# Kernel tuning notes

Hardware: AMD Instinct MI355X
Metric: run time of the kernel (lower is better)

The kernel has to match this reference:

```python
import jax, jax.numpy as jnp
import numpy as np

N_NODES = 10000
N_EDGES = 320000
N_GRAPHS = 64


def _gcn_conv(x, edge_index, W, b, n):
    # PyG GCNConv: add self-loops, symmetric deg^-1/2 normalization, x@W, scatter-add at target, + bias
    loop = jnp.arange(n)
    src = jnp.concatenate([edge_index[0], loop])
    dst = jnp.concatenate([edge_index[1], loop])
    deg = jax.ops.segment_sum(jnp.ones_like(dst, dtype=x.dtype), dst, num_segments=n)
    dinv = jnp.where(deg > 0, 1.0 / jnp.sqrt(jnp.maximum(deg, 1.0)), 0.0)
    norm = dinv[src] * dinv[dst]            # [E']
    h = x @ W                               # [N, out]
    out = jax.ops.segment_sum(h[src] * norm[:, None], dst, num_segments=n)
    return out + b


def _mean_pool(x, batch, g):
    s = jax.ops.segment_sum(x, batch, num_segments=g)
    cnt = jax.ops.segment_sum(jnp.ones((x.shape[0],), x.dtype), batch, num_segments=g)
    return s / jnp.maximum(cnt, 1.0)[:, None]


def setup_inputs() -> dict:
    key = jax.random.key(0)
    ks = jax.random.split(key, 20)
    x = jax.random.normal(ks[0], (N_NODES, 1), dtype=jnp.float32)
    edge_index = jax.random.randint(ks[1], (2, N_EDGES), 0, N_NODES, dtype=jnp.int64)
    batch = jnp.sort(jax.random.randint(ks[2], (N_NODES,), 0, N_GRAPHS, dtype=jnp.int64))

    def lin(k, fi, fo):
        k1, k2 = jax.random.split(k)
        lim = 1.0 / np.sqrt(fi)
        W = jax.random.uniform(k1, (fi, fo), jnp.float32, -lim, lim)
        b = jax.random.uniform(k2, (fo,), jnp.float32, -lim, lim)
        return W, b

    W1, b1 = lin(ks[3], 1, 256)
    W2, b2 = lin(ks[4], 256, 256)
    W3, b3 = lin(ks[5], 256, 128)
    W4, b4 = lin(ks[6], 128, 128)
    W5, b5 = lin(ks[7], 128, 64)
    W6, b6 = lin(ks[8], 64, 32)
    W7, b7 = lin(ks[9], 32, 1)
    return dict(x=x, edge_index=edge_index, batch=batch,
                W1=W1, b1=b1, W2=W2, b2=b2, W3=W3, b3=b3, W4=W4, b4=b4,
                W5=W5, b5=b5, W6=W6, b6=b6, W7=W7, b7=b7)


def reference(x, edge_index, batch, W1, b1, W2, b2, W3, b3, W4, b4, W5, b5, W6, b6, W7, b7):
    n = x.shape[0]
    h = jax.nn.relu(_gcn_conv(x, edge_index, W1, b1, n))
    h = jax.nn.relu(_gcn_conv(h, edge_index, W2, b2, n))
    g = _mean_pool(h, batch, N_GRAPHS)          # [G, 256]
    g = jax.nn.relu(g @ W3 + b3)
    g = jax.nn.relu(g @ W4 + b4)
    g = jax.nn.relu(g @ W5 + b5)
    g = jax.nn.relu(g @ W6 + b6)
    y = (g @ W7 + b7).reshape(-1)               # [G]
    return y
```

## Files before the change

kernel.cpp:

```cpp
#include <hip/hip_runtime.h>

#define N_NODES  10000
#define N_EDGES  320000
#define N_GRAPHS 64
#define F 256
#define POOL_SPLIT 8


__global__ void k_prep(const int* batch, int* cnti, float* s, int* gstart) {
    int i = blockIdx.x * blockDim.x + threadIdx.x;
    if (i >= N_NODES) return;
    cnti[i] = 0;
    s[i] = 0.0f;
    int b = batch[i];
    if (i == 0) {
        for (int g = 0; g <= b; g++) gstart[g] = 0;
    } else {
        int bp = batch[i - 1];
        for (int g = bp + 1; g <= b; g++) gstart[g] = i;
    }
    if (i == N_NODES - 1) {
        for (int g = b + 1; g <= N_GRAPHS; g++) gstart[g] = N_NODES;
    }
}

__global__ void k_deg(const int* dst, int* cnti) {
    int e = blockIdx.x * blockDim.x + threadIdx.x;
    if (e < N_EDGES) atomicAdd(&cnti[dst[e]], 1);
}

__global__ void k_scan(const int* cnti, int* offs, int* cursor, float* dinv) {
    __shared__ int part[256];
    int t = threadIdx.x;
    const int CH = 40;
    int lo = t * CH, hi = lo + CH;
    if (hi > N_NODES) hi = N_NODES;
    if (lo > N_NODES) lo = N_NODES;
    int sum = 0;
    for (int i = lo; i < hi; i++) sum += cnti[i];
    part[t] = sum;
    __syncthreads();
    for (int off = 1; off < 256; off <<= 1) {
        int v = (t >= off) ? part[t - off] : 0;
        __syncthreads();
        if (t >= off) part[t] += v;
        __syncthreads();
    }
    int base = (t == 0) ? 0 : part[t - 1];
    for (int i = lo; i < hi; i++) {
        offs[i] = base; cursor[i] = base; base += cnti[i];
        dinv[i] = 1.0f / sqrtf((float)(cnti[i] + 1));
    }
}

__global__ void k_edge(const int* src, const int* dst, const float* x,
                       const float* dinv, int* cursor, int* csr, float* s) {
    int e = blockIdx.x * blockDim.x + threadIdx.x;
    if (e >= N_EDGES) return;
    int sv = src[e], dv = dst[e];
    int pos = atomicAdd(&cursor[dv], 1);
    csr[pos] = sv;
    atomicAdd(&s[dv], dinv[sv] * x[sv]);
}

__global__ void k_sfin(const float* s, const float* dinv, const float* x, float2* sd) {
    int i = blockIdx.x * blockDim.x + threadIdx.x;
    if (i >= N_NODES) return;
    float di = dinv[i];
    sd[i] = make_float2(di * (s[i] + di * x[i]), di);
}

#define EDGE_TERM(t)                                  \
    acc.x += fmaxf(fmaf((t).x, w.x, bv.x), 0.f) * (t).y; \
    acc.y += fmaxf(fmaf((t).x, w.y, bv.y), 0.f) * (t).y; \
    acc.z += fmaxf(fmaf((t).x, w.z, bv.z), 0.f) * (t).y; \
    acc.w += fmaxf(fmaf((t).x, w.w, bv.w), 0.f) * (t).y;

__global__ __launch_bounds__(256) void k_agg(const float2* sd, const float* W1, const float* b1,
                                             const int* offs, const int* cnti, const int* csr,
                                             float* agg) {
    int wid  = (blockIdx.x * blockDim.x + threadIdx.x) >> 6;
    int lane = threadIdx.x & 63;
    if (wid >= N_NODES) return;
    float4 w  = ((const float4*)W1)[lane];
    float4 bv = ((const float4*)b1)[lane];
    float2 self = sd[wid];
    float4 acc = {0.f, 0.f, 0.f, 0.f};
    EDGE_TERM(self)
    int lo = offs[wid], n = cnti[wid];
    int j = 0;
    for (; j + 3 < n; j += 4) {
        int s0 = csr[lo + j],     s1 = csr[lo + j + 1];
        int s2 = csr[lo + j + 2], s3 = csr[lo + j + 3];
        float2 t0 = sd[s0], t1 = sd[s1], t2 = sd[s2], t3 = sd[s3];
        EDGE_TERM(t0) EDGE_TERM(t1) EDGE_TERM(t2) EDGE_TERM(t3)
    }
    for (; j < n; j++) {
        float2 t = sd[csr[lo + j]];
        EDGE_TERM(t)
    }
    float di = self.y;
    float4 o; o.x = acc.x * di; o.y = acc.y * di; o.z = acc.z * di; o.w = acc.w * di;
    ((float4*)(agg + (size_t)wid * F))[lane] = o;
}

__global__ __launch_bounds__(256) void k_gemm(const float* A, const float* B,
                                              const float* bias, float* C) {
    __shared__ float As[16][68];
    __shared__ float Bs[16][64];
    int tid  = threadIdx.x;
    int row0 = blockIdx.x * 64;
    int col0 = blockIdx.y * 64;
    float acc[4][4] = {};
    int am = tid >> 2, ak = (tid & 3) * 4;
    int bk = tid >> 4, bn = (tid & 15) * 4;
    int ty = tid >> 4, tx = tid & 15;
    for (int k0 = 0; k0 < 256; k0 += 16) {
        float4 av = {0.f, 0.f, 0.f, 0.f};
        if (row0 + am < N_NODES)
            av = *(const float4*)(A + (size_t)(row0 + am) * 256 + k0 + ak);
        As[ak + 0][am] = av.x; As[ak + 1][am] = av.y;
        As[ak + 2][am] = av.z; As[ak + 3][am] = av.w;
        float4 bvv = *(const float4*)(B + (size_t)(k0 + bk) * 256 + col0 + bn);
        *(float4*)&Bs[bk][bn] = bvv;
        __syncthreads();
        #pragma unroll
        for (int k = 0; k < 16; k++) {
            float4 a4 = *(const float4*)&As[k][ty * 4];
            float4 b4 = *(const float4*)&Bs[k][tx * 4];
            float a[4] = {a4.x, a4.y, a4.z, a4.w};
            float b[4] = {b4.x, b4.y, b4.z, b4.w};
            #pragma unroll
            for (int m = 0; m < 4; m++)
                #pragma unroll
                for (int n = 0; n < 4; n++) acc[m][n] += a[m] * b[n];
        }
        __syncthreads();
    }
    #pragma unroll
    for (int m = 0; m < 4; m++) {
        int r = row0 + ty * 4 + m;
        if (r >= N_NODES) continue;
        #pragma unroll
        for (int n = 0; n < 4; n++) {
            int c = col0 + tx * 4 + n;
            C[(size_t)r * 256 + c] = fmaxf(acc[m][n] + bias[c], 0.0f);
        }
    }
}

__global__ void k_pool(const float* out2, const int* gstart, float* partial) {
    int g = blockIdx.x, sp = blockIdx.y, c = threadIdx.x;
    int lo = gstart[g], hi = gstart[g + 1];
    int len = hi - lo;
    int chunk = (len + POOL_SPLIT - 1) / POOL_SPLIT;
    int a = lo + sp * chunk;
    int b = a + chunk; if (b > hi) b = hi;
    float sum = 0.0f;
    for (int i = a; i < b; i++) sum += out2[(size_t)i * F + c];
    partial[((size_t)g * POOL_SPLIT + sp) * F + c] = sum;
}

__global__ void k_head(const float* partial, const int* gstart,
                       const float* W3, const float* b3, const float* W4, const float* b4,
                       const float* W5, const float* b5, const float* W6, const float* b6,
                       const float* W7, const float* b7, float* y) {
    __shared__ float a[256], b[256];
    int g = blockIdx.x, t = threadIdx.x;
    float sum = 0.0f;
    #pragma unroll
    for (int sp = 0; sp < POOL_SPLIT; sp++)
        sum += partial[((size_t)g * POOL_SPLIT + sp) * F + t];
    int cnt = gstart[g + 1] - gstart[g]; if (cnt < 1) cnt = 1;
    a[t] = sum / (float)cnt;
    __syncthreads();
    if (t < 128) { float acc = b3[t]; for (int k = 0; k < 256; k++) acc += a[k] * W3[k * 128 + t]; b[t] = fmaxf(acc, 0.f); }
    __syncthreads();
    if (t < 128) { float acc = b4[t]; for (int k = 0; k < 128; k++) acc += b[k] * W4[k * 128 + t]; a[t] = fmaxf(acc, 0.f); }
    __syncthreads();
    if (t < 64)  { float acc = b5[t]; for (int k = 0; k < 128; k++) acc += a[k] * W5[k * 64 + t];  b[t] = fmaxf(acc, 0.f); }
    __syncthreads();
    if (t < 32)  { float acc = b6[t]; for (int k = 0; k < 64;  k++) acc += b[k] * W6[k * 32 + t];  a[t] = fmaxf(acc, 0.f); }
    __syncthreads();
    if (t == 0)  { float acc = b7[0]; for (int k = 0; k < 32;  k++) acc += a[k] * W7[k]; y[g] = acc; }
}

extern "C" void kernel_launch(void* const* d_in, const int* in_sizes, int n_in,
                              void* d_out, int out_size, void* d_ws, size_t ws_size,
                              hipStream_t stream) {
    const float* x     = (const float*)d_in[0];
    const int*   edges = (const int*)d_in[1];
    const int*   batch = (const int*)d_in[2];
    const float* W1 = (const float*)d_in[3];  const float* b1 = (const float*)d_in[4];
    const float* W2 = (const float*)d_in[5];  const float* b2 = (const float*)d_in[6];
    const float* W3 = (const float*)d_in[7];  const float* b3 = (const float*)d_in[8];
    const float* W4 = (const float*)d_in[9];  const float* b4 = (const float*)d_in[10];
    const float* W5 = (const float*)d_in[11]; const float* b5 = (const float*)d_in[12];
    const float* W6 = (const float*)d_in[13]; const float* b6 = (const float*)d_in[14];
    const float* W7 = (const float*)d_in[15]; const float* b7 = (const float*)d_in[16];
    float* y = (float*)d_out;

    const int* esrc = edges;
    const int* edst = edges + N_EDGES;

    char* w = (char*)d_ws;
    size_t off = 0;
    auto alloc = [&](size_t bytes) { char* p = w + off; off += (bytes + 1023) & ~size_t(1023); return p; };
    int*    cnti    = (int*)   alloc(N_NODES * 4);
    float*  svec    = (float*) alloc(N_NODES * 4);
    int*    offs    = (int*)   alloc(N_NODES * 4);
    int*    cursor  = (int*)   alloc(N_NODES * 4);
    float*  dinv    = (float*) alloc(N_NODES * 4);
    int*    gstart  = (int*)   alloc((N_GRAPHS + 1) * 4);
    int*    csr     = (int*)   alloc(N_EDGES * 4);
    float2* sd      = (float2*)alloc((size_t)N_NODES * 8);
    float*  aggb    = (float*) alloc((size_t)N_NODES * F * 4);
    float*  out2    = (float*) alloc((size_t)N_NODES * F * 4);
    float*  partial = (float*) alloc((size_t)N_GRAPHS * POOL_SPLIT * F * 4);
    (void)ws_size; (void)in_sizes; (void)n_in; (void)out_size;

    const int TB = 256;
    int gbN = (N_NODES + TB - 1) / TB;
    int gbE = (N_EDGES + TB - 1) / TB;

    hipLaunchKernelGGL(k_prep, dim3(gbN), dim3(TB), 0, stream, batch, cnti, svec, gstart);
    hipLaunchKernelGGL(k_deg,  dim3(gbE), dim3(TB), 0, stream, edst, cnti);
    hipLaunchKernelGGL(k_scan, dim3(1),   dim3(TB), 0, stream, cnti, offs, cursor, dinv);
    hipLaunchKernelGGL(k_edge, dim3(gbE), dim3(TB), 0, stream, esrc, edst, x, dinv, cursor, csr, svec);
    hipLaunchKernelGGL(k_sfin, dim3(gbN), dim3(TB), 0, stream, svec, dinv, x, sd);
    hipLaunchKernelGGL(k_agg,  dim3((N_NODES * 64 + TB - 1) / TB), dim3(TB), 0, stream,
                       sd, W1, b1, offs, cnti, csr, aggb);
    hipLaunchKernelGGL(k_gemm, dim3((N_NODES + 63) / 64, 4), dim3(TB), 0, stream,
                       aggb, W2, b2, out2);
    hipLaunchKernelGGL(k_pool, dim3(N_GRAPHS, POOL_SPLIT), dim3(F), 0, stream, out2, gstart, partial);
    hipLaunchKernelGGL(k_head, dim3(N_GRAPHS), dim3(TB), 0, stream,
                       partial, gstart, W3, b3, W4, b4, W5, b5, W6, b6, W7, b7, y);
}
```

Before: 254.9 us.

## Fuse all GCN stages into one persistent cooperative kernel with grid syncs

```diff
diff --git a/kernel.cpp b/kernel.cpp
--- a/kernel.cpp
+++ b/kernel.cpp
@@ -1,17 +1,36 @@
 #include <hip/hip_runtime.h>
+#include <hip/hip_cooperative_groups.h>
+
+namespace cg = cooperative_groups;
 
 #define N_NODES  10000
 #define N_EDGES  320000
 #define N_GRAPHS 64
 #define F 256
-#define POOL_SPLIT 8
-
-
-__global__ void k_prep(const int* batch, int* cnti, float* s, int* gstart) {
-    int i = blockIdx.x * blockDim.x + threadIdx.x;
-    if (i >= N_NODES) return;
-    cnti[i] = 0;
-    s[i] = 0.0f;
+#define NB_MAX 1024
+#define TB 256
+#define POOL_SPLIT 16
+#define NTILES (((N_NODES + 63) / 64) * 4)
+
+
+struct Params {
+    const float* x; const int* esrc; const int* edst; const int* batch;
+    const float *W1, *b1, *W2, *b2, *W3, *b3, *W4, *b4, *W5, *b5, *W6, *b6, *W7, *b7;
+    float* y;
+    int* cnti; float* svec; int* offs; int* cursor; float* dinv; int* gstart;
+    int* csr; float2* sd; float* aggb; float* out2; float* partial;
+};
+
+#define EDGE_TERM(t)                                      \
+    acc.x += fmaxf(fmaf((t).x, w.x, bv.x), 0.f) * (t).y;  \
+    acc.y += fmaxf(fmaf((t).x, w.y, bv.y), 0.f) * (t).y;  \
+    acc.z += fmaxf(fmaf((t).x, w.z, bv.z), 0.f) * (t).y;  \
+    acc.w += fmaxf(fmaf((t).x, w.w, bv.w), 0.f) * (t).y;
+
+
+__device__ __forceinline__ void phase_prep(const int* batch, int* cnti, float* svec,
+                                           int* gstart, int i) {
+    cnti[i] = 0; svec[i] = 0.0f;
     int b = batch[i];
     if (i == 0) {
         for (int g = 0; g <= b; g++) gstart[g] = 0;
@@ -24,66 +43,33 @@
     }
 }
 
-__global__ void k_deg(const int* dst, int* cnti) {
-    int e = blockIdx.x * blockDim.x + threadIdx.x;
-    if (e < N_EDGES) atomicAdd(&cnti[dst[e]], 1);
-}
-
-__global__ void k_scan(const int* cnti, int* offs, int* cursor, float* dinv) {
-    __shared__ int part[256];
-    int t = threadIdx.x;
+__device__ __forceinline__ void phase_scan_block(const int* cnti, int* offs, int* cursor,
+                                                 float* dinv, int* part, int tid) {
     const int CH = 40;
-    int lo = t * CH, hi = lo + CH;
+    int lo = tid * CH, hi = lo + CH;
     if (hi > N_NODES) hi = N_NODES;
     if (lo > N_NODES) lo = N_NODES;
     int sum = 0;
     for (int i = lo; i < hi; i++) sum += cnti[i];
-    part[t] = sum;
+    part[tid] = sum;
     __syncthreads();
     for (int off = 1; off < 256; off <<= 1) {
-        int v = (t >= off) ? part[t - off] : 0;
+        int v = (tid >= off) ? part[tid - off] : 0;
         __syncthreads();
-        if (t >= off) part[t] += v;
+        if (tid >= off) part[tid] += v;
         __syncthreads();
     }
-    int base = (t == 0) ? 0 : part[t - 1];
+    int base = (tid == 0) ? 0 : part[tid - 1];
     for (int i = lo; i < hi; i++) {
         offs[i] = base; cursor[i] = base; base += cnti[i];
         dinv[i] = 1.0f / sqrtf((float)(cnti[i] + 1));
     }
 }
 
-__global__ void k_edge(const int* src, const int* dst, const float* x,
-                       const float* dinv, int* cursor, int* csr, float* s) {
-    int e = blockIdx.x * blockDim.x + threadIdx.x;
-    if (e >= N_EDGES) return;
-    int sv = src[e], dv = dst[e];
-    int pos = atomicAdd(&cursor[dv], 1);
-    csr[pos] = sv;
-    atomicAdd(&s[dv], dinv[sv] * x[sv]);
-}
-
-__global__ void k_sfin(const float* s, const float* dinv, const float* x, float2* sd) {
-    int i = blockIdx.x * blockDim.x + threadIdx.x;
-    if (i >= N_NODES) return;
-    float di = dinv[i];
-    sd[i] = make_float2(di * (s[i] + di * x[i]), di);
-}
-
-#define EDGE_TERM(t)                                  \
-    acc.x += fmaxf(fmaf((t).x, w.x, bv.x), 0.f) * (t).y; \
-    acc.y += fmaxf(fmaf((t).x, w.y, bv.y), 0.f) * (t).y; \
-    acc.z += fmaxf(fmaf((t).x, w.z, bv.z), 0.f) * (t).y; \
-    acc.w += fmaxf(fmaf((t).x, w.w, bv.w), 0.f) * (t).y;
-
-__global__ __launch_bounds__(256) void k_agg(const float2* sd, const float* W1, const float* b1,
-                                             const int* offs, const int* cnti, const int* csr,
-                                             float* agg) {
-    int wid  = (blockIdx.x * blockDim.x + threadIdx.x) >> 6;
-    int lane = threadIdx.x & 63;
-    if (wid >= N_NODES) return;
-    float4 w  = ((const float4*)W1)[lane];
-    float4 bv = ((const float4*)b1)[lane];
+__device__ __forceinline__ void phase_agg_node(const float2* sd, const int* offs,
+                                               const int* cnti, const int* csr,
+                                               float* aggb, int wid, int lane,
+                                               float4 w, float4 bv) {
     float2 self = sd[wid];
     float4 acc = {0.f, 0.f, 0.f, 0.f};
     EDGE_TERM(self)
@@ -101,20 +87,18 @@
     }
     float di = self.y;
     float4 o; o.x = acc.x * di; o.y = acc.y * di; o.z = acc.z * di; o.w = acc.w * di;
-    ((float4*)(agg + (size_t)wid * F))[lane] = o;
-}
-
-__global__ __launch_bounds__(256) void k_gemm(const float* A, const float* B,
-                                              const float* bias, float* C) {
-    __shared__ float As[16][68];
-    __shared__ float Bs[16][64];
-    int tid  = threadIdx.x;
-    int row0 = blockIdx.x * 64;
-    int col0 = blockIdx.y * 64;
-    float acc[4][4] = {};
+    ((float4*)(aggb + (size_t)wid * F))[lane] = o;
+}
+
+__device__ __forceinline__ void phase_gemm_tile(const float* A, const float* B,
+                                                const float* bias, float* C,
+                                                float (*As)[68], float* Bs,
+                                                int t, int tid) {
+    int row0 = (t >> 2) * 64, col0 = (t & 3) * 64;
     int am = tid >> 2, ak = (tid & 3) * 4;
     int bk = tid >> 4, bn = (tid & 15) * 4;
     int ty = tid >> 4, tx = tid & 15;
+    float acc[4][4] = {};
     for (int k0 = 0; k0 < 256; k0 += 16) {
         float4 av = {0.f, 0.f, 0.f, 0.f};
         if (row0 + am < N_NODES)
@@ -122,18 +106,18 @@
         As[ak + 0][am] = av.x; As[ak + 1][am] = av.y;
         As[ak + 2][am] = av.z; As[ak + 3][am] = av.w;
         float4 bvv = *(const float4*)(B + (size_t)(k0 + bk) * 256 + col0 + bn);
-        *(float4*)&Bs[bk][bn] = bvv;
+        *(float4*)&Bs[bk * 64 + bn] = bvv;
         __syncthreads();
         #pragma unroll
         for (int k = 0; k < 16; k++) {
             float4 a4 = *(const float4*)&As[k][ty * 4];
-            float4 b4 = *(const float4*)&Bs[k][tx * 4];
+            float4 b4 = *(const float4*)&Bs[k * 64 + tx * 4];
             float a[4] = {a4.x, a4.y, a4.z, a4.w};
             float b[4] = {b4.x, b4.y, b4.z, b4.w};
             #pragma unroll
             for (int m = 0; m < 4; m++)
                 #pragma unroll
-                for (int n = 0; n < 4; n++) acc[m][n] += a[m] * b[n];
+                for (int n2 = 0; n2 < 4; n2++) acc[m][n2] += a[m] * b[n2];
         }
         __syncthreads();
     }
@@ -142,97 +126,222 @@
         int r = row0 + ty * 4 + m;
         if (r >= N_NODES) continue;
         #pragma unroll
-        for (int n = 0; n < 4; n++) {
-            int c = col0 + tx * 4 + n;
-            C[(size_t)r * 256 + c] = fmaxf(acc[m][n] + bias[c], 0.0f);
+        for (int n2 = 0; n2 < 4; n2++) {
+            int c = col0 + tx * 4 + n2;
+            C[(size_t)r * 256 + c] = fmaxf(acc[m][n2] + bias[c], 0.0f);
         }
     }
 }
 
-__global__ void k_pool(const float* out2, const int* gstart, float* partial) {
-    int g = blockIdx.x, sp = blockIdx.y, c = threadIdx.x;
-    int lo = gstart[g], hi = gstart[g + 1];
+__device__ __forceinline__ void phase_head_graph(const Params& p, int g, int tid,
+                                                 float* ha, float* hb) {
+    float sum = 0.0f;
+    #pragma unroll
+    for (int sp = 0; sp < POOL_SPLIT; sp++)
+        sum += p.partial[((size_t)g * POOL_SPLIT + sp) * F + tid];
+    int cnt = p.gstart[g + 1] - p.gstart[g]; if (cnt < 1) cnt = 1;
+    ha[tid] = sum / (float)cnt;
+    __syncthreads();
+    if (tid < 128) { float acc = p.b3[tid]; for (int k = 0; k < 256; k++) acc += ha[k] * p.W3[k * 128 + tid]; hb[tid] = fmaxf(acc, 0.f); }
+    __syncthreads();
+    if (tid < 128) { float acc = p.b4[tid]; for (int k = 0; k < 128; k++) acc += hb[k] * p.W4[k * 128 + tid]; ha[tid] = fmaxf(acc, 0.f); }
+    __syncthreads();
+    if (tid < 64)  { float acc = p.b5[tid]; for (int k = 0; k < 128; k++) acc += ha[k] * p.W5[k * 64 + tid];  hb[tid] = fmaxf(acc, 0.f); }
+    __syncthreads();
+    if (tid < 32)  { float acc = p.b6[tid]; for (int k = 0; k < 64;  k++) acc += hb[k] * p.W6[k * 32 + tid];  ha[tid] = fmaxf(acc, 0.f); }
+    __syncthreads();
+    if (tid == 0)  { float acc = p.b7[0]; for (int k = 0; k < 32;  k++) acc += ha[k] * p.W7[k]; p.y[g] = acc; }
+}
+
+
+__global__ __launch_bounds__(TB, 4) void k_all(Params p) {
+    cg::grid_group grid = cg::this_grid();
+    const int bid = blockIdx.x, tid = threadIdx.x;
+    const int nb = gridDim.x;
+    const int nthreads = nb * TB;
+    const int gtid = bid * TB + tid;
+    __shared__ float smem[16 * 68 + 16 * 64];
+
+    for (int i = gtid; i < N_NODES; i += nthreads)
+        phase_prep(p.batch, p.cnti, p.svec, p.gstart, i);
+    grid.sync();
+
+    for (int e = gtid; e < N_EDGES; e += nthreads) atomicAdd(&p.cnti[p.edst[e]], 1);
+    grid.sync();
+
+    if (bid == 0)
+        phase_scan_block(p.cnti, p.offs, p.cursor, p.dinv, (int*)smem, tid);
+    grid.sync();
+
+    for (int e = gtid; e < N_EDGES; e += nthreads) {
+        int sv = p.esrc[e], dv = p.edst[e];
+        int pos = atomicAdd(&p.cursor[dv], 1);
+        p.csr[pos] = sv;
+        atomicAdd(&p.svec[dv], p.dinv[sv] * p.x[sv]);
+    }
+    grid.sync();
+
+    for (int i = gtid; i < N_NODES; i += nthreads) {
+        float di = p.dinv[i];
+        p.sd[i] = make_float2(di * (p.svec[i] + di * p.x[i]), di);
+    }
+    grid.sync();
+
+    {
+        const int lane = tid & 63;
+        const int totWaves = nthreads >> 6;
+        float4 w  = ((const float4*)p.W1)[lane];
+        float4 bv = ((const float4*)p.b1)[lane];
+        for (int wid = gtid >> 6; wid < N_NODES; wid += totWaves)
+            phase_agg_node(p.sd, p.offs, p.cnti, p.csr, p.aggb, wid, lane, w, bv);
+    }
+    grid.sync();
+
+    {
+        float (*As)[68] = (float(*)[68])smem;
+        float* Bs = smem + 16 * 68;
+        for (int t = bid; t < NTILES; t += nb)
+            phase_gemm_tile(p.aggb, p.W2, p.b2, p.out2, As, Bs, t, tid);
+    }
+    grid.sync();
+
+    for (int item = bid; item < N_GRAPHS * POOL_SPLIT; item += nb) {
+        int g = item >> 4, sp = item & 15;
+        int lo = p.gstart[g], hi = p.gstart[g + 1];
+        int len = hi - lo;
+        int chunk = (len + POOL_SPLIT - 1) / POOL_SPLIT;
+        int a = lo + sp * chunk;
+        int b = a + chunk; if (b > hi) b = hi;
+        float sum = 0.0f;
+        for (int i = a; i < b; i++) sum += p.out2[(size_t)i * F + tid];
+        p.partial[(size_t)item * F + tid] = sum;
+    }
+    grid.sync();
+
+    for (int g = bid; g < N_GRAPHS; g += nb)
+        phase_head_graph(p, g, tid, smem, smem + 256);
+}
+
+
+__global__ void f_prep(Params p) {
+    int i = blockIdx.x * blockDim.x + threadIdx.x;
+    if (i < N_NODES) phase_prep(p.batch, p.cnti, p.svec, p.gstart, i);
+}
+__global__ void f_deg(Params p) {
+    int e = blockIdx.x * blockDim.x + threadIdx.x;
+    if (e < N_EDGES) atomicAdd(&p.cnti[p.edst[e]], 1);
+}
+__global__ void f_scan(Params p) {
+    __shared__ int part[256];
+    phase_scan_block(p.cnti, p.offs, p.cursor, p.dinv, part, threadIdx.x);
+}
+__global__ void f_edge(Params p) {
+    int e = blockIdx.x * blockDim.x + threadIdx.x;
+    if (e >= N_EDGES) return;
+    int sv = p.esrc[e], dv = p.edst[e];
+    int pos = atomicAdd(&p.cursor[dv], 1);
+    p.csr[pos] = sv;
+    atomicAdd(&p.svec[dv], p.dinv[sv] * p.x[sv]);
+}
+__global__ void f_sfin(Params p) {
+    int i = blockIdx.x * blockDim.x + threadIdx.x;
+    if (i >= N_NODES) return;
+    float di = p.dinv[i];
+    p.sd[i] = make_float2(di * (p.svec[i] + di * p.x[i]), di);
+}
+__global__ __launch_bounds__(256) void f_agg(Params p) {
+    int wid  = (blockIdx.x * blockDim.x + threadIdx.x) >> 6;
+    int lane = threadIdx.x & 63;
+    if (wid >= N_NODES) return;
+    float4 w  = ((const float4*)p.W1)[lane];
+    float4 bv = ((const float4*)p.b1)[lane];
+    phase_agg_node(p.sd, p.offs, p.cnti, p.csr, p.aggb, wid, lane, w, bv);
+}
+__global__ __launch_bounds__(256) void f_gemm(Params p) {
+    __shared__ float smem[16 * 68 + 16 * 64];
+    phase_gemm_tile(p.aggb, p.W2, p.b2, p.out2, (float(*)[68])smem, smem + 16 * 68,
+                    blockIdx.x, threadIdx.x);
+}
+__global__ void f_pool(Params p) {
+    int item = blockIdx.x;
+    int g = item >> 4, sp = item & 15, tid = threadIdx.x;
+    int lo = p.gstart[g], hi = p.gstart[g + 1];
     int len = hi - lo;
     int chunk = (len + POOL_SPLIT - 1) / POOL_SPLIT;
     int a = lo + sp * chunk;
     int b = a + chunk; if (b > hi) b = hi;
     float sum = 0.0f;
-    for (int i = a; i < b; i++) sum += out2[(size_t)i * F + c];
-    partial[((size_t)g * POOL_SPLIT + sp) * F + c] = sum;
-}
-
-__global__ void k_head(const float* partial, const int* gstart,
-                       const float* W3, const float* b3, const float* W4, const float* b4,
-                       const float* W5, const float* b5, const float* W6, const float* b6,
-                       const float* W7, const float* b7, float* y) {
-    __shared__ float a[256], b[256];
-    int g = blockIdx.x, t = threadIdx.x;
-    float sum = 0.0f;
-    #pragma unroll
-    for (int sp = 0; sp < POOL_SPLIT; sp++)
-        sum += partial[((size_t)g * POOL_SPLIT + sp) * F + t];
-    int cnt = gstart[g + 1] - gstart[g]; if (cnt < 1) cnt = 1;
-    a[t] = sum / (float)cnt;
-    __syncthreads();
-    if (t < 128) { float acc = b3[t]; for (int k = 0; k < 256; k++) acc += a[k] * W3[k * 128 + t]; b[t] = fmaxf(acc, 0.f); }
-    __syncthreads();
-    if (t < 128) { float acc = b4[t]; for (int k = 0; k < 128; k++) acc += b[k] * W4[k * 128 + t]; a[t] = fmaxf(acc, 0.f); }
-    __syncthreads();
-    if (t < 64)  { float acc = b5[t]; for (int k = 0; k < 128; k++) acc += a[k] * W5[k * 64 + t];  b[t] = fmaxf(acc, 0.f); }
-    __syncthreads();
-    if (t < 32)  { float acc = b6[t]; for (int k = 0; k < 64;  k++) acc += b[k] * W6[k * 32 + t];  a[t] = fmaxf(acc, 0.f); }
-    __syncthreads();
-    if (t == 0)  { float acc = b7[0]; for (int k = 0; k < 32;  k++) acc += a[k] * W7[k]; y[g] = acc; }
+    for (int i = a; i < b; i++) sum += p.out2[(size_t)i * F + tid];
+    p.partial[(size_t)item * F + tid] = sum;
+}
+__global__ void f_head(Params p) {
+    __shared__ float smem[512];
+    phase_head_graph(p, blockIdx.x, threadIdx.x, smem, smem + 256);
 }
 
 extern "C" void kernel_launch(void* const* d_in, const int* in_sizes, int n_in,
                               void* d_out, int out_size, void* d_ws, size_t ws_size,
                               hipStream_t stream) {
-    const float* x     = (const float*)d_in[0];
-    const int*   edges = (const int*)d_in[1];
-    const int*   batch = (const int*)d_in[2];
-    const float* W1 = (const float*)d_in[3];  const float* b1 = (const float*)d_in[4];
-    const float* W2 = (const float*)d_in[5];  const float* b2 = (const float*)d_in[6];
-    const float* W3 = (const float*)d_in[7];  const float* b3 = (const float*)d_in[8];
-    const float* W4 = (const float*)d_in[9];  const float* b4 = (const float*)d_in[10];
-    const float* W5 = (const float*)d_in[11]; const float* b5 = (const float*)d_in[12];
-    const float* W6 = (const float*)d_in[13]; const float* b6 = (const float*)d_in[14];
-    const float* W7 = (const float*)d_in[15]; const float* b7 = (const float*)d_in[16];
-    float* y = (float*)d_out;
-
-    const int* esrc = edges;
-    const int* edst = edges + N_EDGES;
+    Params P;
+    P.x     = (const float*)d_in[0];
+    P.esrc  = (const int*)d_in[1];
+    P.edst  = ((const int*)d_in[1]) + N_EDGES;
+    P.batch = (const int*)d_in[2];
+    P.W1 = (const float*)d_in[3];  P.b1 = (const float*)d_in[4];
+    P.W2 = (const float*)d_in[5];  P.b2 = (const float*)d_in[6];
+    P.W3 = (const float*)d_in[7];  P.b3 = (const float*)d_in[8];
+    P.W4 = (const float*)d_in[9];  P.b4 = (const float*)d_in[10];
+    P.W5 = (const float*)d_in[11]; P.b5 = (const float*)d_in[12];
+    P.W6 = (const float*)d_in[13]; P.b6 = (const float*)d_in[14];
+    P.W7 = (const float*)d_in[15]; P.b7 = (const float*)d_in[16];
+    P.y  = (float*)d_out;
 
     char* w = (char*)d_ws;
     size_t off = 0;
-    auto alloc = [&](size_t bytes) { char* p = w + off; off += (bytes + 1023) & ~size_t(1023); return p; };
-    int*    cnti    = (int*)   alloc(N_NODES * 4);
-    float*  svec    = (float*) alloc(N_NODES * 4);
-    int*    offs    = (int*)   alloc(N_NODES * 4);
-    int*    cursor  = (int*)   alloc(N_NODES * 4);
-    float*  dinv    = (float*) alloc(N_NODES * 4);
-    int*    gstart  = (int*)   alloc((N_GRAPHS + 1) * 4);
-    int*    csr     = (int*)   alloc(N_EDGES * 4);
-    float2* sd      = (float2*)alloc((size_t)N_NODES * 8);
-    float*  aggb    = (float*) alloc((size_t)N_NODES * F * 4);
-    float*  out2    = (float*) alloc((size_t)N_NODES * F * 4);
-    float*  partial = (float*) alloc((size_t)N_GRAPHS * POOL_SPLIT * F * 4);
+    auto alloc = [&](size_t bytes) { char* q = w + off; off += (bytes + 1023) & ~size_t(1023); return q; };
+    P.cnti    = (int*)   alloc(N_NODES * 4);
+    P.svec    = (float*) alloc(N_NODES * 4);
+    P.offs    = (int*)   alloc(N_NODES * 4);
+    P.cursor  = (int*)   alloc(N_NODES * 4);
+    P.dinv    = (float*) alloc(N_NODES * 4);
+    P.gstart  = (int*)   alloc((N_GRAPHS + 1) * 4);
+    P.csr     = (int*)   alloc(N_EDGES * 4);
+    P.sd      = (float2*)alloc((size_t)N_NODES * 8);
+    P.aggb    = (float*) alloc((size_t)N_NODES * F * 4);
+    P.out2    = (float*) alloc((size_t)N_NODES * F * 4);
+    P.partial = (float*) alloc((size_t)N_GRAPHS * POOL_SPLIT * F * 4);
     (void)ws_size; (void)in_sizes; (void)n_in; (void)out_size;
 
-    const int TB = 256;
-    int gbN = (N_NODES + TB - 1) / TB;
-    int gbE = (N_EDGES + TB - 1) / TB;
-
-    hipLaunchKernelGGL(k_prep, dim3(gbN), dim3(TB), 0, stream, batch, cnti, svec, gstart);
-    hipLaunchKernelGGL(k_deg,  dim3(gbE), dim3(TB), 0, stream, edst, cnti);
-    hipLaunchKernelGGL(k_scan, dim3(1),   dim3(TB), 0, stream, cnti, offs, cursor, dinv);
-    hipLaunchKernelGGL(k_edge, dim3(gbE), dim3(TB), 0, stream, esrc, edst, x, dinv, cursor, csr, svec);
-    hipLaunchKernelGGL(k_sfin, dim3(gbN), dim3(TB), 0, stream, svec, dinv, x, sd);
-    hipLaunchKernelGGL(k_agg,  dim3((N_NODES * 64 + TB - 1) / TB), dim3(TB), 0, stream,
-                       sd, W1, b1, offs, cnti, csr, aggb);
-    hipLaunchKernelGGL(k_gemm, dim3((N_NODES + 63) / 64, 4), dim3(TB), 0, stream,
-                       aggb, W2, b2, out2);
-    hipLaunchKernelGGL(k_pool, dim3(N_GRAPHS, POOL_SPLIT), dim3(F), 0, stream, out2, gstart, partial);
-    hipLaunchKernelGGL(k_head, dim3(N_GRAPHS), dim3(TB), 0, stream,
-                       partial, gstart, W3, b3, W4, b4, W5, b5, W6, b6, W7, b7, y);
-}
+    int dev = 0, coopOK = 0, nCU = 256, bpc = 0;
+    hipGetDevice(&dev);
+    hipDeviceGetAttribute(&coopOK, hipDeviceAttributeCooperativeLaunch, dev);
+    hipDeviceGetAttribute(&nCU, hipDeviceAttributeMultiprocessorCount, dev);
+    hipOccupancyMaxActiveBlocksPerMultiprocessor(&bpc, (const void*)k_all, TB, 0);
+    if (bpc < 0) bpc = 0;
+    long long nbll = (long long)bpc * (long long)nCU;
+    int nb = (nbll > NB_MAX) ? NB_MAX : (int)nbll;
+
+    bool launched = false;
+    if (coopOK && nb >= 64) {
+        void* args[] = { &P };
+        hipError_t err = hipLaunchCooperativeKernel((const void*)k_all,
+                                                    dim3(nb), dim3(TB), args, 0, stream);
+        launched = (err == hipSuccess);
+        if (!launched) (void)hipGetLastError();
+    }
+
+    if (!launched) {
+        const int TBf = 256;
+        int gbN = (N_NODES + TBf - 1) / TBf;
+        int gbE = (N_EDGES + TBf - 1) / TBf;
+        hipLaunchKernelGGL(f_prep, dim3(gbN), dim3(TBf), 0, stream, P);
+        hipLaunchKernelGGL(f_deg,  dim3(gbE), dim3(TBf), 0, stream, P);
+        hipLaunchKernelGGL(f_scan, dim3(1),   dim3(TBf), 0, stream, P);
+        hipLaunchKernelGGL(f_edge, dim3(gbE), dim3(TBf), 0, stream, P);
+        hipLaunchKernelGGL(f_sfin, dim3(gbN), dim3(TBf), 0, stream, P);
+        hipLaunchKernelGGL(f_agg,  dim3((N_NODES * 64 + TBf - 1) / TBf), dim3(TBf), 0, stream, P);
+        hipLaunchKernelGGL(f_gemm, dim3(NTILES), dim3(TBf), 0, stream, P);
+        hipLaunchKernelGGL(f_pool, dim3(N_GRAPHS * POOL_SPLIT), dim3(TBf), 0, stream, P);
+        hipLaunchKernelGGL(f_head, dim3(N_GRAPHS), dim3(TBf), 0, stream, P);
+    }
+}
```

New measurement: 734.0 us. 2.88x slower.

## Fuse scan, finalize, and head into preceding kernels via last-block-done counters

Applied to the files above, without the earlier changes.

```diff
diff --git a/kernel.cpp b/kernel.cpp
--- a/kernel.cpp
+++ b/kernel.cpp
@@ -4,117 +4,126 @@
 #define N_EDGES  320000
 #define N_GRAPHS 64
 #define F 256
-#define POOL_SPLIT 8
-
-
-__global__ void k_prep(const int* batch, int* cnti, float* s, int* gstart) {
-    int i = blockIdx.x * blockDim.x + threadIdx.x;
-    if (i >= N_NODES) return;
-    cnti[i] = 0;
-    s[i] = 0.0f;
-    int b = batch[i];
-    if (i == 0) {
-        for (int g = 0; g <= b; g++) gstart[g] = 0;
-    } else {
-        int bp = batch[i - 1];
-        for (int g = bp + 1; g <= b; g++) gstart[g] = i;
-    }
-    if (i == N_NODES - 1) {
-        for (int g = b + 1; g <= N_GRAPHS; g++) gstart[g] = N_NODES;
-    }
-}
-
-__global__ void k_deg(const int* dst, int* cnti) {
-    int e = blockIdx.x * blockDim.x + threadIdx.x;
-    if (e < N_EDGES) atomicAdd(&cnti[dst[e]], 1);
-}
-
-__global__ void k_scan(const int* cnti, int* offs, int* cursor, float* dinv) {
+#define POOL_SPLIT 16
+#define NTILES (((N_NODES + 63) / 64) * 4)
+#define EDGE_BLOCKS (N_EDGES / 256)
+
+
+struct Params {
+    const float* x; const int* esrc; const int* edst; const int* batch;
+    const float *W1, *b1, *W2, *b2, *W3, *b3, *W4, *b4, *W5, *b5, *W6, *b6, *W7, *b7;
+    float* y;
+    int* cnti; float* svec; float* gacc; int* deg_ctr; int* edge_ctr; int* hsync;
+    int* offs; int* cursor; float* dinv; int* gstart;
+    int* csr; float2* sd; float* aggb; float* out2;
+};
+
+#define EDGE_TERM(t)                                      \
+    acc.x += fmaxf(fmaf((t).x, w.x, bv.x), 0.f) * (t).y;  \
+    acc.y += fmaxf(fmaf((t).x, w.y, bv.y), 0.f) * (t).y;  \
+    acc.z += fmaxf(fmaf((t).x, w.z, bv.z), 0.f) * (t).y;  \
+    acc.w += fmaxf(fmaf((t).x, w.w, bv.w), 0.f) * (t).y;
+
+__global__ __launch_bounds__(256) void k_deg(Params p) {
+    const int tid = threadIdx.x;
+    int e = blockIdx.x * 256 + tid;
+    atomicAdd(&p.cnti[p.edst[e]], 1);
+    __threadfence();
+    __shared__ int isLast;
     __shared__ int part[256];
-    int t = threadIdx.x;
+    if (tid == 0) isLast = (atomicAdd(p.deg_ctr, 1) == (int)gridDim.x - 1);
+    __syncthreads();
+    if (!isLast) return;
     const int CH = 40;
-    int lo = t * CH, hi = lo + CH;
+    int lo = tid * CH, hi = lo + CH;
     if (hi > N_NODES) hi = N_NODES;
     if (lo > N_NODES) lo = N_NODES;
     int sum = 0;
-    for (int i = lo; i < hi; i++) sum += cnti[i];
-    part[t] = sum;
+    for (int i = lo; i < hi; i++) sum += atomicAdd(&p.cnti[i], 0);
+    part[tid] = sum;
     __syncthreads();
     for (int off = 1; off < 256; off <<= 1) {
-        int v = (t >= off) ? part[t - off] : 0;
-        __syncthreads();
-        if (t >= off) part[t] += v;
-        __syncthreads();
-    }
-    int base = (t == 0) ? 0 : part[t - 1];
+        int v = (tid >= off) ? part[tid - off] : 0;
+        __syncthreads();
+        if (tid >= off) part[tid] += v;
+        __syncthreads();
+    }
+    int base = (tid == 0) ? 0 : part[tid - 1];
     for (int i = lo; i < hi; i++) {
-        offs[i] = base; cursor[i] = base; base += cnti[i];
-        dinv[i] = 1.0f / sqrtf((float)(cnti[i] + 1));
-    }
-}
-
-__global__ void k_edge(const int* src, const int* dst, const float* x,
-                       const float* dinv, int* cursor, int* csr, float* s) {
-    int e = blockIdx.x * blockDim.x + threadIdx.x;
-    if (e >= N_EDGES) return;
-    int sv = src[e], dv = dst[e];
-    int pos = atomicAdd(&cursor[dv], 1);
-    csr[pos] = sv;
-    atomicAdd(&s[dv], dinv[sv] * x[sv]);
-}
-
-__global__ void k_sfin(const float* s, const float* dinv, const float* x, float2* sd) {
-    int i = blockIdx.x * blockDim.x + threadIdx.x;
-    if (i >= N_NODES) return;
-    float di = dinv[i];
-    sd[i] = make_float2(di * (s[i] + di * x[i]), di);
-}
-
-#define EDGE_TERM(t)                                  \
-    acc.x += fmaxf(fmaf((t).x, w.x, bv.x), 0.f) * (t).y; \
-    acc.y += fmaxf(fmaf((t).x, w.y, bv.y), 0.f) * (t).y; \
-    acc.z += fmaxf(fmaf((t).x, w.z, bv.z), 0.f) * (t).y; \
-    acc.w += fmaxf(fmaf((t).x, w.w, bv.w), 0.f) * (t).y;
-
-__global__ __launch_bounds__(256) void k_agg(const float2* sd, const float* W1, const float* b1,
-                                             const int* offs, const int* cnti, const int* csr,
-                                             float* agg) {
-    int wid  = (blockIdx.x * blockDim.x + threadIdx.x) >> 6;
+        int c = atomicAdd(&p.cnti[i], 0);
+        p.offs[i] = base; p.cursor[i] = base; base += c;
+        p.dinv[i] = 1.0f / sqrtf((float)(c + 1));
+    }
+    for (int i = lo; i < hi; i++) {
+        int b = p.batch[i];
+        if (i == 0) {
+            for (int g = 0; g <= b; g++) p.gstart[g] = 0;
+        } else {
+            int bp = p.batch[i - 1];
+            for (int g = bp + 1; g <= b; g++) p.gstart[g] = i;
+        }
+        if (i == N_NODES - 1) {
+            for (int g = b + 1; g <= N_GRAPHS; g++) p.gstart[g] = N_NODES;
+        }
+    }
+}
+
+__global__ __launch_bounds__(256) void k_edge(Params p) {
+    const int tid = threadIdx.x;
+    int e = blockIdx.x * 256 + tid;
+    int sv = p.esrc[e], dv = p.edst[e];
+    int pos = atomicAdd(&p.cursor[dv], 1);
+    p.csr[pos] = sv;
+    atomicAdd(&p.svec[dv], p.dinv[sv] * p.x[sv]);
+    __threadfence();
+    __shared__ int isLast;
+    if (tid == 0) isLast = (atomicAdd(p.edge_ctr, 1) == (int)gridDim.x - 1);
+    __syncthreads();
+    if (!isLast) return;
+    for (int i = tid; i < N_NODES; i += 256) {
+        float s = atomicAdd(&p.svec[i], 0.0f);
+        float di = p.dinv[i];
+        p.sd[i] = make_float2(di * (s + di * p.x[i]), di);
+    }
+}
+
+__global__ __launch_bounds__(256) void k_agg(Params p) {
+    int wid  = (blockIdx.x * 256 + threadIdx.x) >> 6;
     int lane = threadIdx.x & 63;
     if (wid >= N_NODES) return;
-    float4 w  = ((const float4*)W1)[lane];
-    float4 bv = ((const float4*)b1)[lane];
-    float2 self = sd[wid];
+    float4 w  = ((const float4*)p.W1)[lane];
+    float4 bv = ((const float4*)p.b1)[lane];
+    float2 self = p.sd[wid];
     float4 acc = {0.f, 0.f, 0.f, 0.f};
     EDGE_TERM(self)
-    int lo = offs[wid], n = cnti[wid];
+    int lo = p.offs[wid], n = p.cnti[wid];
     int j = 0;
     for (; j + 3 < n; j += 4) {
-        int s0 = csr[lo + j],     s1 = csr[lo + j + 1];
-        int s2 = csr[lo + j + 2], s3 = csr[lo + j + 3];
-        float2 t0 = sd[s0], t1 = sd[s1], t2 = sd[s2], t3 = sd[s3];
+        int s0 = p.csr[lo + j],     s1 = p.csr[lo + j + 1];
+        int s2 = p.csr[lo + j + 2], s3 = p.csr[lo + j + 3];
+        float2 t0 = p.sd[s0], t1 = p.sd[s1], t2 = p.sd[s2], t3 = p.sd[s3];
         EDGE_TERM(t0) EDGE_TERM(t1) EDGE_TERM(t2) EDGE_TERM(t3)
     }
     for (; j < n; j++) {
-        float2 t = sd[csr[lo + j]];
+        float2 t = p.sd[p.csr[lo + j]];
         EDGE_TERM(t)
     }
     float di = self.y;
     float4 o; o.x = acc.x * di; o.y = acc.y * di; o.z = acc.z * di; o.w = acc.w * di;
-    ((float4*)(agg + (size_t)wid * F))[lane] = o;
-}
-
-__global__ __launch_bounds__(256) void k_gemm(const float* A, const float* B,
-                                              const float* bias, float* C) {
+    ((float4*)(p.aggb + (size_t)wid * F))[lane] = o;
+}
+
+__global__ __launch_bounds__(256) void k_gemm(Params p) {
     __shared__ float As[16][68];
     __shared__ float Bs[16][64];
+    const float* A = p.aggb;
+    const float* B = p.W2;
     int tid  = threadIdx.x;
-    int row0 = blockIdx.x * 64;
-    int col0 = blockIdx.y * 64;
-    float acc[4][4] = {};
+    int row0 = (blockIdx.x >> 2) * 64, col0 = (blockIdx.x & 3) * 64;
     int am = tid >> 2, ak = (tid & 3) * 4;
     int bk = tid >> 4, bn = (tid & 15) * 4;
     int ty = tid >> 4, tx = tid & 15;
+    float acc[4][4] = {};
     for (int k0 = 0; k0 < 256; k0 += 16) {
         float4 av = {0.f, 0.f, 0.f, 0.f};
         if (row0 + am < N_NODES)
@@ -133,7 +142,7 @@
             #pragma unroll
             for (int m = 0; m < 4; m++)
                 #pragma unroll
-                for (int n = 0; n < 4; n++) acc[m][n] += a[m] * b[n];
+                for (int n2 = 0; n2 < 4; n2++) acc[m][n2] += a[m] * b[n2];
         }
         __syncthreads();
     }
@@ -142,97 +151,87 @@
         int r = row0 + ty * 4 + m;
         if (r >= N_NODES) continue;
         #pragma unroll
-        for (int n = 0; n < 4; n++) {
-            int c = col0 + tx * 4 + n;
-            C[(size_t)r * 256 + c] = fmaxf(acc[m][n] + bias[c], 0.0f);
-        }
-    }
-}
-
-__global__ void k_pool(const float* out2, const int* gstart, float* partial) {
-    int g = blockIdx.x, sp = blockIdx.y, c = threadIdx.x;
-    int lo = gstart[g], hi = gstart[g + 1];
+        for (int n2 = 0; n2 < 4; n2++) {
+            int c = col0 + tx * 4 + n2;
+            p.out2[(size_t)r * 256 + c] = fmaxf(acc[m][n2] + p.b2[c], 0.0f);
+        }
+    }
+}
+
+__global__ __launch_bounds__(256) void k_poolhead(Params p) {
+    const int g = blockIdx.x >> 4, sp = blockIdx.x & 15, tid = threadIdx.x;
+    int lo = p.gstart[g], hi = p.gstart[g + 1];
     int len = hi - lo;
     int chunk = (len + POOL_SPLIT - 1) / POOL_SPLIT;
     int a = lo + sp * chunk;
     int b = a + chunk; if (b > hi) b = hi;
     float sum = 0.0f;
-    for (int i = a; i < b; i++) sum += out2[(size_t)i * F + c];
-    partial[((size_t)g * POOL_SPLIT + sp) * F + c] = sum;
-}
-
-__global__ void k_head(const float* partial, const int* gstart,
-                       const float* W3, const float* b3, const float* W4, const float* b4,
-                       const float* W5, const float* b5, const float* W6, const float* b6,
-                       const float* W7, const float* b7, float* y) {
-    __shared__ float a[256], b[256];
-    int g = blockIdx.x, t = threadIdx.x;
-    float sum = 0.0f;
-    #pragma unroll
-    for (int sp = 0; sp < POOL_SPLIT; sp++)
-        sum += partial[((size_t)g * POOL_SPLIT + sp) * F + t];
-    int cnt = gstart[g + 1] - gstart[g]; if (cnt < 1) cnt = 1;
-    a[t] = sum / (float)cnt;
-    __syncthreads();
-    if (t < 128) { float acc = b3[t]; for (int k = 0; k < 256; k++) acc += a[k] * W3[k * 128 + t]; b[t] = fmaxf(acc, 0.f); }
-    __syncthreads();
-    if (t < 128) { float acc = b4[t]; for (int k = 0; k < 128; k++) acc += b[k] * W4[k * 128 + t]; a[t] = fmaxf(acc, 0.f); }
-    __syncthreads();
-    if (t < 64)  { float acc = b5[t]; for (int k = 0; k < 128; k++) acc += a[k] * W5[k * 64 + t];  b[t] = fmaxf(acc, 0.f); }
-    __syncthreads();
-    if (t < 32)  { float acc = b6[t]; for (int k = 0; k < 64;  k++) acc += b[k] * W6[k * 32 + t];  a[t] = fmaxf(acc, 0.f); }
-    __syncthreads();
-    if (t == 0)  { float acc = b7[0]; for (int k = 0; k < 32;  k++) acc += a[k] * W7[k]; y[g] = acc; }
+    for (int i = a; i < b; i++) sum += p.out2[(size_t)i * F + tid];
+    atomicAdd(&p.gacc[g * F + tid], sum);
+    __threadfence();
+    __shared__ int isLast;
+    if (tid == 0) isLast = (atomicAdd(&p.hsync[g], 1) == POOL_SPLIT - 1);
+    __syncthreads();
+    if (!isLast) return;
+    __shared__ float ha[256], hb[256];
+    float gv = atomicAdd(&p.gacc[g * F + tid], 0.0f);
+    int cnt = (len < 1) ? 1 : len;
+    ha[tid] = gv / (float)cnt;
+    __syncthreads();
+    if (tid < 128) { float acc = p.b3[tid]; for (int k = 0; k < 256; k++) acc += ha[k] * p.W3[k * 128 + tid]; hb[tid] = fmaxf(acc, 0.f); }
+    __syncthreads();
+    if (tid < 128) { float acc = p.b4[tid]; for (int k = 0; k < 128; k++) acc += hb[k] * p.W4[k * 128 + tid]; ha[tid] = fmaxf(acc, 0.f); }
+    __syncthreads();
+    if (tid < 64)  { float acc = p.b5[tid]; for (int k = 0; k < 128; k++) acc += ha[k] * p.W5[k * 64 + tid];  hb[tid] = fmaxf(acc, 0.f); }
+    __syncthreads();
+    if (tid < 32)  { float acc = p.b6[tid]; for (int k = 0; k < 64;  k++) acc += hb[k] * p.W6[k * 32 + tid];  ha[tid] = fmaxf(acc, 0.f); }
+    __syncthreads();
+    if (tid == 0)  { float acc = p.b7[0]; for (int k = 0; k < 32;  k++) acc += ha[k] * p.W7[k]; p.y[g] = acc; }
 }
 
 extern "C" void kernel_launch(void* const* d_in, const int* in_sizes, int n_in,
                               void* d_out, int out_size, void* d_ws, size_t ws_size,
                               hipStream_t stream) {
-    const float* x     = (const float*)d_in[0];
-    const int*   edges = (const int*)d_in[1];
-    const int*   batch = (const int*)d_in[2];
-    const float* W1 = (const float*)d_in[3];  const float* b1 = (const float*)d_in[4];
-    const float* W2 = (const float*)d_in[5];  const float* b2 = (const float*)d_in[6];
-    const float* W3 = (const float*)d_in[7];  const float* b3 = (const float*)d_in[8];
-    const float* W4 = (const float*)d_in[9];  const float* b4 = (const float*)d_in[10];
-    const float* W5 = (const float*)d_in[11]; const float* b5 = (const float*)d_in[12];
-    const float* W6 = (const float*)d_in[13]; const float* b6 = (const float*)d_in[14];
-    const float* W7 = (const float*)d_in[15]; const float* b7 = (const float*)d_in[16];
-    float* y = (float*)d_out;
-
-    const int* esrc = edges;
-    const int* edst = edges + N_EDGES;
-
-    char* w = (char*)d_ws;
+    Params P;
+    P.x     = (const float*)d_in[0];
+    P.esrc  = (const int*)d_in[1];
+    P.edst  = ((const int*)d_in[1]) + N_EDGES;
+    P.batch = (const int*)d_in[2];
+    P.W1 = (const float*)d_in[3];  P.b1 = (const float*)d_in[4];
+    P.W2 = (const float*)d_in[5];  P.b2 = (const float*)d_in[6];
+    P.W3 = (const float*)d_in[7];  P.b3 = (const float*)d_in[8];
+    P.W4 = (const float*)d_in[9];  P.b4 = (const float*)d_in[10];
+    P.W5 = (const float*)d_in[11]; P.b5 = (const float*)d_in[12];
+    P.W6 = (const float*)d_in[13]; P.b6 = (const float*)d_in[14];
+    P.W7 = (const float*)d_in[15]; P.b7 = (const float*)d_in[16];
+    P.y  = (float*)d_out;
+
+    char* z = (char*)d_ws;
+    P.cnti     = (int*)  (z + 0);
+    P.svec     = (float*)(z + 160000);
+    P.gacc     = (float*)(z + 320000);
+    P.deg_ctr  = (int*)  (z + 385536);
+    P.edge_ctr = (int*)  (z + 385540);
+    P.hsync    = (int*)  (z + 385544);
+    const size_t zbytes = 385800;
+
+    char* w = z + ((zbytes + 1023) & ~size_t(1023));
     size_t off = 0;
-    auto alloc = [&](size_t bytes) { char* p = w + off; off += (bytes + 1023) & ~size_t(1023); return p; };
-    int*    cnti    = (int*)   alloc(N_NODES * 4);
-    float*  svec    = (float*) alloc(N_NODES * 4);
-    int*    offs    = (int*)   alloc(N_NODES * 4);
-    int*    cursor  = (int*)   alloc(N_NODES * 4);
-    float*  dinv    = (float*) alloc(N_NODES * 4);
-    int*    gstart  = (int*)   alloc((N_GRAPHS + 1) * 4);
-    int*    csr     = (int*)   alloc(N_EDGES * 4);
-    float2* sd      = (float2*)alloc((size_t)N_NODES * 8);
-    float*  aggb    = (float*) alloc((size_t)N_NODES * F * 4);
-    float*  out2    = (float*) alloc((size_t)N_NODES * F * 4);
-    float*  partial = (float*) alloc((size_t)N_GRAPHS * POOL_SPLIT * F * 4);
+    auto alloc = [&](size_t bytes) { char* q = w + off; off += (bytes + 1023) & ~size_t(1023); return q; };
+    P.offs   = (int*)   alloc(N_NODES * 4);
+    P.cursor = (int*)   alloc(N_NODES * 4);
+    P.dinv   = (float*) alloc(N_NODES * 4);
+    P.gstart = (int*)   alloc((N_GRAPHS + 1) * 4);
+    P.csr    = (int*)   alloc(N_EDGES * 4);
+    P.sd     = (float2*)alloc((size_t)N_NODES * 8);
+    P.aggb   = (float*) alloc((size_t)N_NODES * F * 4);
+    P.out2   = (float*) alloc((size_t)N_NODES * F * 4);
     (void)ws_size; (void)in_sizes; (void)n_in; (void)out_size;
 
-    const int TB = 256;
-    int gbN = (N_NODES + TB - 1) / TB;
-    int gbE = (N_EDGES + TB - 1) / TB;
-
-    hipLaunchKernelGGL(k_prep, dim3(gbN), dim3(TB), 0, stream, batch, cnti, svec, gstart);
-    hipLaunchKernelGGL(k_deg,  dim3(gbE), dim3(TB), 0, stream, edst, cnti);
-    hipLaunchKernelGGL(k_scan, dim3(1),   dim3(TB), 0, stream, cnti, offs, cursor, dinv);
-    hipLaunchKernelGGL(k_edge, dim3(gbE), dim3(TB), 0, stream, esrc, edst, x, dinv, cursor, csr, svec);
-    hipLaunchKernelGGL(k_sfin, dim3(gbN), dim3(TB), 0, stream, svec, dinv, x, sd);
-    hipLaunchKernelGGL(k_agg,  dim3((N_NODES * 64 + TB - 1) / TB), dim3(TB), 0, stream,
-                       sd, W1, b1, offs, cnti, csr, aggb);
-    hipLaunchKernelGGL(k_gemm, dim3((N_NODES + 63) / 64, 4), dim3(TB), 0, stream,
-                       aggb, W2, b2, out2);
-    hipLaunchKernelGGL(k_pool, dim3(N_GRAPHS, POOL_SPLIT), dim3(F), 0, stream, out2, gstart, partial);
-    hipLaunchKernelGGL(k_head, dim3(N_GRAPHS), dim3(TB), 0, stream,
-                       partial, gstart, W3, b3, W4, b4, W5, b5, W6, b6, W7, b7, y);
-}
+    hipMemsetAsync(z, 0, zbytes, stream);
+    hipLaunchKernelGGL(k_deg,      dim3(EDGE_BLOCKS), dim3(256), 0, stream, P);
+    hipLaunchKernelGGL(k_edge,     dim3(EDGE_BLOCKS), dim3(256), 0, stream, P);
+    hipLaunchKernelGGL(k_agg,      dim3((N_NODES * 64) / 256 + 1), dim3(256), 0, stream, P);
+    hipLaunchKernelGGL(k_gemm,     dim3(NTILES), dim3(256), 0, stream, P);
+    hipLaunchKernelGGL(k_poolhead, dim3(N_GRAPHS * POOL_SPLIT), dim3(256), 0, stream, P);
+}
```

Result: slower. 522.9 us (+105.1%).
